# Performance work log

Measured on AMD Instinct MI355X. Metric: run time of the kernel, lower is better.

Reference implementation:

```python
import jax, jax.numpy as jnp
import numpy as np

N_AGENTS = 8
HID = 256            # hidden_size == comm_dim
COMP = 32            # composition_dim
VOCAB = 256          # vocab_size (table has VOCAB+1 rows, last row = EOS token)
T = HID // COMP      # total_tokens = 8
EPSILON = 1e-6
NF = 1.0 / np.sqrt(HID)  # norm_factor


def setup_inputs() -> dict:
    key = jax.random.key(0)
    ks = jax.random.split(key, 12)
    B = 2048 * N_AGENTS  # n_rollout_threads * num_agents
    s = 0.05
    return {
        "hidden_state": jax.random.normal(ks[0], (B, HID), jnp.float32),
        "eps": jax.random.normal(ks[1], (T, B, COMP), jnp.float32),
        "W_Q": jax.random.normal(ks[2], (HID, HID), jnp.float32) * s,
        "b_Q": jnp.zeros((HID,), jnp.float32),
        "W_K": jax.random.normal(ks[3], (HID, HID), jnp.float32) * s,
        "b_K": jnp.zeros((HID,), jnp.float32),
        "W_mu": jax.random.normal(ks[4], (HID, COMP), jnp.float32) * s,
        "b_mu": jnp.zeros((COMP,), jnp.float32),
        "W_var": jax.random.normal(ks[5], (HID, COMP), jnp.float32) * s,
        "b_var": jnp.zeros((COMP,), jnp.float32),
        "vocab": jax.random.uniform(ks[6], (VOCAB + 1, COMP), jnp.float32, minval=-2.0, maxval=2.0),
        "W_sum": jax.random.normal(ks[7], (HID, HID), jnp.float32) * s,
        "b_sum": jnp.zeros((HID,), jnp.float32),
        "W_head": jax.random.normal(ks[8], (HID, HID), jnp.float32) * s,
        "b_head": jnp.zeros((HID,), jnp.float32),
    }


def _forward(hidden_state, eps, W_Q, b_Q, W_K, b_K, W_mu, b_mu, W_var, b_var,
             vocab, W_sum, b_sum, W_head, b_head):
    B = hidden_state.shape[0]
    # NOTE: original code sets V = to_K(hidden_state) (to_V is unused) -- kept faithfully.
    Q = (hidden_state @ W_Q + b_Q) * NF            # [B, HID]
    V = hidden_state @ W_K + b_K                   # [B, HID]
    EOS = vocab[-1]                                # [COMP]

    message = jnp.zeros((B, T, COMP), hidden_state.dtype)
    mask = jnp.ones((B,), hidden_state.dtype)
    finished = jnp.zeros((B,), bool)

    # Sequential recurrence over a small fixed number of tokens (T = 8).
    for i in range(T):
        m = message.reshape(B, HID)
        K = (m @ W_K + b_K) * NF                   # [B, HID]
        attn = jax.nn.softmax(-(Q * K), axis=-1)   # softmin == softmax of negated logits
        hidden_attn = attn * V                     # [B, HID]
        token_mu = hidden_attn @ W_mu + b_mu       # [B, COMP]
        token_log_var = hidden_attn @ W_var + b_var
        token = eps[i] * jnp.exp(0.5 * token_log_var) + token_mu
        # per-dimension min of squared distance over all vocab entries (faithful to torch.min(.,1)[0])
        token = jnp.min((token[:, None, :] - vocab) ** 2, axis=1)  # [B, COMP]
        token = token * mask[:, None]
        eos_hit = jnp.sum((token - EOS) ** 2, axis=-1) < EPSILON   # [B]
        if i > 0:
            prev_hit = jnp.any(
                jnp.sum((token[:, None, :] - message[:, :i]) ** 2, axis=-1) < EPSILON, axis=1)
            hit = jnp.logical_or(prev_hit, eos_hit)
        else:
            hit = eos_hit
        new_eos = jnp.logical_and(hit, jnp.logical_not(finished))
        token = jnp.where(new_eos[:, None], EOS, token)
        mask = jnp.where(hit, jnp.zeros_like(mask), mask)
        finished = jnp.logical_or(finished, hit)
        message = message.at[:, i].set(token)

    comm = message.reshape(B, HID)                 # comm_dim == HID
    b = B // N_AGENTS
    comm = comm.reshape(b, N_AGENTS, HID) / (N_AGENTS - 1)  # comm_mode 'avg'
    # expand to [b, n, n, C] then sum over dim 1 == broadcast total sum to every agent
    comm_sum = jnp.broadcast_to(comm.sum(axis=1, keepdims=True), (b, N_AGENTS, HID))
    comm_sum = comm_sum.reshape(B, HID)
    out = comm_sum @ W_sum + b_sum                 # comm_sum_head
    out = jax.nn.relu(out @ W_head + b_head)       # active_func(comm_head(.))
    return out


def reference(hidden_state, eps, W_Q, b_Q, W_K, b_K, W_mu, b_mu, W_var, b_var,
              vocab, W_sum, b_sum, W_head, b_head):
    return _forward(hidden_state, eps, W_Q, b_Q, W_K, b_K, W_mu, b_mu, W_var, b_var,
                    vocab, W_sum, b_sum, W_head, b_head)
```

## Files before the change

kernel.cpp:

```cpp
#include <hip/hip_runtime.h>

#define ROWSB 32
#define HIDN 256
#define TT 8
#define EPSI 1e-6f
#define HAS 260
#define SVS 260
#define TBSTR 40
#define NCELL 128
#define WS_LUT_F   (32*SVS)
#define WS_DINFO_F (32*SVS + 2048)
#define WS_WMV_F   (32*SVS + 2048 + 64)

__device__ __forceinline__ void ld4(float* d, const float* p) {
  float4 v = *(const float4*)p;
  d[0] = v.x; d[1] = v.y; d[2] = v.z; d[3] = v.w;
}
__device__ __forceinline__ void ld2(float* d, const float* p) {
  float2 v = *(const float2*)p;
  d[0] = v.x; d[1] = v.y;
}
__device__ __forceinline__ void lds_fence() {
  asm volatile("s_waitcnt lgkmcnt(0)" ::: "memory");
}
__device__ __forceinline__ void fma8(float4 wv, float h0, float h1,
                                     float* mu0, float* lv0, float* mu1, float* lv1) {
  mu0[0] += h0*wv.x; lv0[0] += h0*wv.y; mu0[1] += h0*wv.z; lv0[1] += h0*wv.w;
  mu1[0] += h1*wv.x; lv1[0] += h1*wv.y; mu1[1] += h1*wv.z; lv1[1] += h1*wv.w;
}

__global__ __launch_bounds__(256)
void sort_vocab(const float* __restrict__ vocab,
                const float* __restrict__ Wmu, const float* __restrict__ Wvar,
                float* __restrict__ ws) {
  __shared__ float arr[512];
  const int d = blockIdx.x;
  const int t = threadIdx.x;
  ws[WS_WMV_F + ((size_t)t*32 + d)*2 + 0] = Wmu[(size_t)t*32 + d];
  ws[WS_WMV_F + ((size_t)t*32 + d)*2 + 1] = Wvar[(size_t)t*32 + d];
  arr[t] = (t < 257) ? vocab[t*32 + d] : 3.0e38f;
  arr[t+256] = (t == 0) ? vocab[256*32 + d] : 3.0e38f;
  __syncthreads();
  for (int k = 2; k <= 512; k <<= 1) {
    for (int j = k >> 1; j > 0; j >>= 1) {
      #pragma unroll
      for (int h = 0; h < 2; ++h) {
        int i = t + h*256;
        int ixj = i ^ j;
        if (ixj > i) {
          float a = arr[i], b = arr[ixj];
          bool up = ((i & k) == 0);
          if ((a > b) == up) { arr[i] = b; arr[ixj] = a; }
        }
      }
      __syncthreads();
    }
  }
  #pragma unroll
  for (int h = 0; h < 2; ++h) {
    int i = t + h*256;
    if (i < SVS) ws[d*SVS + i] = (i < 257) ? arr[i] : 3.0e38f;
  }
  float base = arr[0];
  float maxv = arr[256];
  float scale = (float)NCELL / fmaxf(maxv - base, 1e-30f);
  if (t == 0) {
    float2* dinfo = (float2*)(ws + WS_DINFO_F);
    dinfo[d] = make_float2(base, scale);
  }
  if (t < NCELL) {
    float target = base + (float)t * (maxv - base) * (1.0f/(float)NCELL);
    int lo = 0, hi = 257;
    while (lo < hi) { int mid = (lo+hi)>>1; if (arr[mid] < target) lo = mid+1; else hi = mid; }
    ((unsigned short*)(ws + WS_LUT_F))[d*NCELL + t] = (unsigned short)lo;
  }
}

__global__ __launch_bounds__(256, 2)
void mac_fused(const float* __restrict__ hs, const float* __restrict__ eps,
               const float* __restrict__ WQ, const float* __restrict__ bQ,
               const float* __restrict__ WK, const float* __restrict__ bK,
               const float* __restrict__ Wmu, const float* __restrict__ bmu,
               const float* __restrict__ Wvar, const float* __restrict__ bvar,
               const float* __restrict__ vocab,
               const float* __restrict__ Wsum, const float* __restrict__ bsum,
               const float* __restrict__ Whead, const float* __restrict__ bhead,
               const float* __restrict__ ws, float* __restrict__ out, int Btot)
{
  __shared__ __align__(16) float ha[ROWSB*HAS];
  __shared__ __align__(16) float sV[32*SVS];
  __shared__ __align__(16) unsigned short lut[32*NCELL];
  __shared__ __align__(16) float tokbuf[ROWSB*TBSTR];
  __shared__ float ivbuf[ROWSB], finbuf[ROWSB];

  const int t   = threadIdx.x;
  const int c4  = t & 63;
  const int w   = t >> 6;
  const int rp  = t >> 4;
  const int dp  = t & 15;
  const int d0u = (c4 << 2) & 31;
  const int tg  = c4 >> 3;
  const int rowbase = blockIdx.x * ROWSB;

  float Qr[8][4], Vr[8][4], Kr[8][4], MSGr[8][4];
  float eosv[4];
  unsigned fin = 0u;

  {
    const float* hp = hs + (size_t)(rowbase + w*8)*HIDN + c4*4;
    #pragma unroll
    for (int rr = 0; rr < 8; ++rr)
      *(float4*)&ha[(w*8+rr)*HAS + c4*4] = *(const float4*)(hp + (size_t)rr*HIDN);
  }
  for (int i = t; i < 32*SVS/4; i += 256)
    *(float4*)&sV[i*4] = *(const float4*)(ws + (size_t)i*4);
  for (int i = t; i < 512; i += 256)
    ((float4*)lut)[i] = ((const float4*)(ws + WS_LUT_F))[i];
  if (c4 < 8) finbuf[w*8 + c4] = 0.f;
  ld4(eosv, vocab + 256*32 + d0u);
  {
    float bq[4], bk[4];
    ld4(bq, bQ + c4*4); ld4(bk, bK + c4*4);
    #pragma unroll
    for (int rr = 0; rr < 8; ++rr) {
      #pragma unroll
      for (int k = 0; k < 4; ++k) { Qr[rr][k] = bq[k]; Vr[rr][k] = bk[k]; }
    }
  }
  float dbr[2], dsr[2];
  {
    float t0[4];
    ld4(t0, ws + WS_DINFO_F + dp*4);
    dbr[0]=t0[0]; dsr[0]=t0[1]; dbr[1]=t0[2]; dsr[1]=t0[3];
  }
  float bm[2], bv[2];
  ld2(bm, bmu + dp*2); ld2(bv, bvar + dp*2);
  lds_fence();

  #pragma unroll 2
  for (int jq = 0; jq < 64; ++jq) {
    float hsq[8][4];
    #pragma unroll
    for (int rr = 0; rr < 8; ++rr) ld4(hsq[rr], &ha[(w*8+rr)*HAS + jq*4]);
    #pragma unroll
    for (int m = 0; m < 4; ++m) {
      float wq[4], wk[4];
      ld4(wq, WQ + (size_t)(jq*4+m)*HIDN + c4*4);
      ld4(wk, WK + (size_t)(jq*4+m)*HIDN + c4*4);
      #pragma unroll
      for (int rr = 0; rr < 8; ++rr) {
        #pragma unroll
        for (int k = 0; k < 4; ++k) {
          Qr[rr][k] += hsq[rr][m]*wq[k];
          Vr[rr][k] += hsq[rr][m]*wk[k];
        }
      }
    }
  }
  {
    float bk[4]; ld4(bk, bK + c4*4);
    #pragma unroll
    for (int rr = 0; rr < 8; ++rr) {
      #pragma unroll
      for (int k = 0; k < 4; ++k) {
        Qr[rr][k] *= (1.0f/256.0f);
        Kr[rr][k]   = bk[k];
        MSGr[rr][k] = 0.f;
      }
    }
  }

  __syncthreads();

  for (int it = 0; it < TT; ++it) {
    if (it > 0) {
      const float* Wr = WK + (size_t)((it-1)*32)*HIDN + c4*4;
      #pragma unroll 2
      for (int cq = 0; cq < 8; ++cq) {
        float tq[8][4];
        #pragma unroll
        for (int rr = 0; rr < 8; ++rr) ld4(tq[rr], &tokbuf[(w*8+rr)*TBSTR + cq*4]);
        #pragma unroll
        for (int m = 0; m < 4; ++m) {
          float wv[4]; ld4(wv, Wr + (size_t)(cq*4+m)*HIDN);
          #pragma unroll
          for (int rr = 0; rr < 8; ++rr) {
            #pragma unroll
            for (int k = 0; k < 4; ++k) Kr[rr][k] += tq[rr][m]*wv[k];
          }
        }
      }
    }

    float ep0[2], ep1[2];
    ld2(ep0, eps + ((size_t)it*Btot + rowbase + 2*rp)*32 + dp*2);
    ld2(ep1, eps + ((size_t)it*Btot + rowbase + 2*rp+1)*32 + dp*2);

    #pragma unroll
    for (int rr = 0; rr < 8; ++rr) {
      float e[4]; float s = 0.f;
      #pragma unroll
      for (int k = 0; k < 4; ++k) { e[k] = __expf(-(Qr[rr][k]*Kr[rr][k])); s += e[k]; }
      #pragma unroll
      for (int off = 32; off >= 1; off >>= 1) s += __shfl_xor(s, off);
      if (c4 == rr) ivbuf[w*8+rr] = 1.0f / s;
      *(float4*)&ha[(w*8+rr)*HAS + c4*4] =
          make_float4(e[0]*Vr[rr][0], e[1]*Vr[rr][1], e[2]*Vr[rr][2], e[3]*Vr[rr][3]);
    }
    lds_fence();

    float mu0[2]={0,0}, lv0[2]={0,0}, mu1[2]={0,0}, lv1[2]={0,0};
    {
      const float* wmv  = ws + WS_WMV_F + dp*4;
      const float* har0 = &ha[(2*rp)*HAS];
      const float* har1 = &ha[(2*rp+1)*HAS];
      float4 wb0[8], wb1[8];
      #pragma unroll
      for (int u = 0; u < 8; ++u) wb0[u] = *(const float4*)(wmv + (size_t)u*64);
      #pragma unroll 1
      for (int bb = 0; bb < 16; ++bb) {
        {
          const int b = 2*bb;
          float4 h0a = *(const float4*)(har0 + b*8);
          float4 h1a = *(const float4*)(har1 + b*8);
          float4 h0b = *(const float4*)(har0 + b*8 + 4);
          float4 h1b = *(const float4*)(har1 + b*8 + 4);
          const float* wp = wmv + (size_t)(b+1)*512;
          #pragma unroll
          for (int u = 0; u < 8; ++u) wb1[u] = *(const float4*)(wp + (size_t)u*64);
          fma8(wb0[0], h0a.x, h1a.x, mu0, lv0, mu1, lv1);
          fma8(wb0[1], h0a.y, h1a.y, mu0, lv0, mu1, lv1);
          fma8(wb0[2], h0a.z, h1a.z, mu0, lv0, mu1, lv1);
          fma8(wb0[3], h0a.w, h1a.w, mu0, lv0, mu1, lv1);
          fma8(wb0[4], h0b.x, h1b.x, mu0, lv0, mu1, lv1);
          fma8(wb0[5], h0b.y, h1b.y, mu0, lv0, mu1, lv1);
          fma8(wb0[6], h0b.z, h1b.z, mu0, lv0, mu1, lv1);
          fma8(wb0[7], h0b.w, h1b.w, mu0, lv0, mu1, lv1);
        }
        {
          const int b = 2*bb+1;
          float4 h0a = *(const float4*)(har0 + b*8);
          float4 h1a = *(const float4*)(har1 + b*8);
          float4 h0b = *(const float4*)(har0 + b*8 + 4);
          float4 h1b = *(const float4*)(har1 + b*8 + 4);
          if (bb < 15) {
            const float* wp = wmv + (size_t)(b+1)*512;
            #pragma unroll
            for (int u = 0; u < 8; ++u) wb0[u] = *(const float4*)(wp + (size_t)u*64);
          }
          fma8(wb1[0], h0a.x, h1a.x, mu0, lv0, mu1, lv1);
          fma8(wb1[1], h0a.y, h1a.y, mu0, lv0, mu1, lv1);
          fma8(wb1[2], h0a.z, h1a.z, mu0, lv0, mu1, lv1);
          fma8(wb1[3], h0a.w, h1a.w, mu0, lv0, mu1, lv1);
          fma8(wb1[4], h0b.x, h1b.x, mu0, lv0, mu1, lv1);
          fma8(wb1[5], h0b.y, h1b.y, mu0, lv0, mu1, lv1);
          fma8(wb1[6], h0b.z, h1b.z, mu0, lv0, mu1, lv1);
          fma8(wb1[7], h0b.w, h1b.w, mu0, lv0, mu1, lv1);
        }
      }
    }
    {
      float ivr0 = ivbuf[2*rp],  ivr1 = ivbuf[2*rp+1];
      float msk0 = 1.0f - finbuf[2*rp], msk1 = 1.0f - finbuf[2*rp+1];
      float md0[2], md1[2];
      #pragma unroll
      for (int d = 0; d < 2; ++d) {
        const int dim = 2*dp + d;
        const float* sp = &sV[dim*SVS];
        {
          float mu = mu0[d]*ivr0 + bm[d];
          float lv = lv0[d]*ivr0 + bv[d];
          float x  = ep0[d]*__expf(0.5f*lv) + mu;
          int c = (int)((x - dbr[d]) * dsr[d]);
          c = min(max(c, 0), NCELL-1);
          int idx = (int)lut[dim*NCELL + c];
          float v = sp[idx];
          while (v < x) { ++idx; v = sp[idx]; }
          float dn = v - x;
          float dpv = (idx > 0) ? (x - sp[idx-1]) : 3.0e38f;
          md0[d] = fminf(dn, dpv);
        }
        {
          float mu = mu1[d]*ivr1 + bm[d];
          float lv = lv1[d]*ivr1 + bv[d];
          float x  = ep1[d]*__expf(0.5f*lv) + mu;
          int c = (int)((x - dbr[d]) * dsr[d]);
          c = min(max(c, 0), NCELL-1);
          int idx = (int)lut[dim*NCELL + c];
          float v = sp[idx];
          while (v < x) { ++idx; v = sp[idx]; }
          float dn = v - x;
          float dpv = (idx > 0) ? (x - sp[idx-1]) : 3.0e38f;
          md1[d] = fminf(dn, dpv);
        }
      }
      *(float2*)&tokbuf[(2*rp)*TBSTR + dp*2]   = make_float2(md0[0]*md0[0]*msk0, md0[1]*md0[1]*msk0);
      *(float2*)&tokbuf[(2*rp+1)*TBSTR + dp*2] = make_float2(md1[0]*md1[0]*msk1, md1[1]*md1[1]*msk1);
    }
    lds_fence();

    {
      float tokr[8][4];
      #pragma unroll
      for (int rr = 0; rr < 8; ++rr) ld4(tokr[rr], &tokbuf[(w*8+rr)*TBSTR + d0u]);
      unsigned newfin = fin;
      #pragma unroll
      for (int rr = 0; rr < 8; ++rr) {
        float pd = 0.f, ed = 0.f;
        #pragma unroll
        for (int k = 0; k < 4; ++k) { float dm = tokr[rr][k]-MSGr[rr][k]; pd += dm*dm; }
        if (tg == 0) {
          #pragma unroll
          for (int k = 0; k < 4; ++k) { float de = tokr[rr][k]-eosv[k]; ed += de*de; }
        }
        pd += __shfl_xor(pd, 1); ed += __shfl_xor(ed, 1);
        pd += __shfl_xor(pd, 2); ed += __shfl_xor(ed, 2);
        pd += __shfl_xor(pd, 4); ed += __shfl_xor(ed, 4);
        bool lane_hit = (tg < it && pd < EPSI) || (tg == 0 && ed < EPSI);
        bool hit = (__ballot(lane_hit) != 0ull);
        if (hit) {
          if ((tg == it) && !((fin >> rr) & 1u)) {
            #pragma unroll
            for (int k = 0; k < 4; ++k) tokr[rr][k] = eosv[k];
          }
          newfin |= (1u << rr);
        }
        if (tg == it) {
          #pragma unroll
          for (int k = 0; k < 4; ++k) MSGr[rr][k] = tokr[rr][k];
        }
      }
      if (tg == it) {
        #pragma unroll
        for (int rr = 0; rr < 8; ++rr)
          *(float4*)&tokbuf[(w*8+rr)*TBSTR + d0u] =
              make_float4(MSGr[rr][0], MSGr[rr][1], MSGr[rr][2], MSGr[rr][3]);
      }
      if (c4 < 8) finbuf[w*8+c4] = ((newfin >> c4) & 1u) ? 1.f : 0.f;
      fin = newfin;
    }
    lds_fence();
  }

  __syncthreads();
  float* commb = ha;
  float* o1    = ha + 4*HAS;
  {
    float cs[4] = {0,0,0,0};
    #pragma unroll
    for (int rr = 0; rr < 8; ++rr) {
      #pragma unroll
      for (int k = 0; k < 4; ++k) cs[k] += MSGr[rr][k];
    }
    const float i7 = 1.0f/7.0f;
    *(float4*)&commb[w*HAS + c4*4] = make_float4(cs[0]*i7, cs[1]*i7, cs[2]*i7, cs[3]*i7);
  }
  __syncthreads();
  {
    float bs = bsum[t];
    float a1[4] = {bs, bs, bs, bs};
    #pragma unroll 2
    for (int jq = 0; jq < 64; ++jq) {
      float w4[4];
      #pragma unroll
      for (int m = 0; m < 4; ++m) w4[m] = Wsum[(size_t)(jq*4+m)*HIDN + t];
      #pragma unroll
      for (int g = 0; g < 4; ++g) {
        float c[4]; ld4(c, &commb[g*HAS + jq*4]);
        a1[g] += c[0]*w4[0] + c[1]*w4[1] + c[2]*w4[2] + c[3]*w4[3];
      }
    }
    #pragma unroll
    for (int g = 0; g < 4; ++g) o1[g*HAS + t] = a1[g];
  }
  __syncthreads();
  {
    float bh = bhead[t];
    float a2[4] = {bh, bh, bh, bh};
    #pragma unroll 2
    for (int jq = 0; jq < 64; ++jq) {
      float w4[4];
      #pragma unroll
      for (int m = 0; m < 4; ++m) w4[m] = Whead[(size_t)(jq*4+m)*HIDN + t];
      #pragma unroll
      for (int g = 0; g < 4; ++g) {
        float c[4]; ld4(c, &o1[g*HAS + jq*4]);
        a2[g] += c[0]*w4[0] + c[1]*w4[1] + c[2]*w4[2] + c[3]*w4[3];
      }
    }
    #pragma unroll
    for (int g = 0; g < 4; ++g) {
      float r = fmaxf(a2[g], 0.f);
      #pragma unroll
      for (int rr = 0; rr < 8; ++rr)
        out[(size_t)(rowbase + g*8 + rr)*HIDN + t] = r;
    }
  }
}

extern "C" void kernel_launch(void* const* d_in, const int* in_sizes, int n_in,
                              void* d_out, int out_size, void* d_ws, size_t ws_size,
                              hipStream_t stream) {
    const float* hs    = (const float*)d_in[0];
    const float* eps   = (const float*)d_in[1];
    const float* WQ    = (const float*)d_in[2];
    const float* bQ    = (const float*)d_in[3];
    const float* WK    = (const float*)d_in[4];
    const float* bK    = (const float*)d_in[5];
    const float* Wmu   = (const float*)d_in[6];
    const float* bmu   = (const float*)d_in[7];
    const float* Wvar  = (const float*)d_in[8];
    const float* bvar  = (const float*)d_in[9];
    const float* vocab = (const float*)d_in[10];
    const float* Wsum  = (const float*)d_in[11];
    const float* bsum  = (const float*)d_in[12];
    const float* Whead = (const float*)d_in[13];
    const float* bhead = (const float*)d_in[14];
    float* o = (float*)d_out;
    float* wsf = (float*)d_ws;
    int Btot = in_sizes[0] / HIDN;
    hipLaunchKernelGGL(sort_vocab, dim3(32), dim3(256), 0, stream, vocab, Wmu, Wvar, wsf);
    hipLaunchKernelGGL(mac_fused, dim3(Btot / ROWSB), dim3(256), 0, stream,
                       hs, eps, WQ, bQ, WK, bK, Wmu, bmu, Wvar, bvar,
                       vocab, Wsum, bsum, Whead, bhead, wsf, o, Btot);
}
```

Before: 424.8 us.

## Move sorted vocab and LUT to global memory, spill V to LDS

The per-block shared copies of the sorted vocab columns and the lookup table are dropped, and the nearest-neighbour search now reads them from global memory (cache-resident). The LUT grows from 128 to 512 cells so the linear scan after the lookup is shorter. The V projection is no longer held in registers across the recurrence; it is written to a new LDS buffer and reloaded each iteration, which frees registers. A __syncthreads is replaced by an lgkmcnt wait. The aim is lower register and LDS pressure and higher occupancy, at the cost of global-memory latency in the search loop and extra LDS traffic.

```diff
diff --git a/kernel.cpp b/kernel.cpp
--- a/kernel.cpp
+++ b/kernel.cpp
@@ -7,10 +7,10 @@
 #define HAS 260
 #define SVS 260
 #define TBSTR 40
-#define NCELL 128
+#define NCELL 512
 #define WS_LUT_F   (32*SVS)
-#define WS_DINFO_F (32*SVS + 2048)
-#define WS_WMV_F   (32*SVS + 2048 + 64)
+#define WS_DINFO_F (32*SVS + 8192)
+#define WS_WMV_F   (32*SVS + 8192 + 64)
 
 __device__ __forceinline__ void ld4(float* d, const float* p) {
   float4 v = *(const float4*)p;
@@ -68,11 +68,13 @@
     float2* dinfo = (float2*)(ws + WS_DINFO_F);
     dinfo[d] = make_float2(base, scale);
   }
-  if (t < NCELL) {
-    float target = base + (float)t * (maxv - base) * (1.0f/(float)NCELL);
+  #pragma unroll
+  for (int h = 0; h < 2; ++h) {
+    int cell = t + h*256;
+    float target = base + (float)cell * (maxv - base) * (1.0f/(float)NCELL);
     int lo = 0, hi = 257;
     while (lo < hi) { int mid = (lo+hi)>>1; if (arr[mid] < target) lo = mid+1; else hi = mid; }
-    ((unsigned short*)(ws + WS_LUT_F))[d*NCELL + t] = (unsigned short)lo;
+    ((unsigned short*)(ws + WS_LUT_F))[d*NCELL + cell] = (unsigned short)lo;
   }
 }
 
@@ -88,8 +90,7 @@
                const float* __restrict__ ws, float* __restrict__ out, int Btot)
 {
   __shared__ __align__(16) float ha[ROWSB*HAS];
-  __shared__ __align__(16) float sV[32*SVS];
-  __shared__ __align__(16) unsigned short lut[32*NCELL];
+  __shared__ __align__(16) float vbuf[ROWSB*HAS];
   __shared__ __align__(16) float tokbuf[ROWSB*TBSTR];
   __shared__ float ivbuf[ROWSB], finbuf[ROWSB];
 
@@ -102,7 +103,7 @@
   const int tg  = c4 >> 3;
   const int rowbase = blockIdx.x * ROWSB;
 
-  float Qr[8][4], Vr[8][4], Kr[8][4], MSGr[8][4];
+  float Qr[8][4], Kr[8][4], MSGr[8][4];
   float eosv[4];
   unsigned fin = 0u;
 
@@ -112,21 +113,8 @@
     for (int rr = 0; rr < 8; ++rr)
       *(float4*)&ha[(w*8+rr)*HAS + c4*4] = *(const float4*)(hp + (size_t)rr*HIDN);
   }
-  for (int i = t; i < 32*SVS/4; i += 256)
-    *(float4*)&sV[i*4] = *(const float4*)(ws + (size_t)i*4);
-  for (int i = t; i < 512; i += 256)
-    ((float4*)lut)[i] = ((const float4*)(ws + WS_LUT_F))[i];
   if (c4 < 8) finbuf[w*8 + c4] = 0.f;
   ld4(eosv, vocab + 256*32 + d0u);
-  {
-    float bq[4], bk[4];
-    ld4(bq, bQ + c4*4); ld4(bk, bK + c4*4);
-    #pragma unroll
-    for (int rr = 0; rr < 8; ++rr) {
-      #pragma unroll
-      for (int k = 0; k < 4; ++k) { Qr[rr][k] = bq[k]; Vr[rr][k] = bk[k]; }
-    }
-  }
   float dbr[2], dsr[2];
   {
     float t0[4];
@@ -137,25 +125,41 @@
   ld2(bm, bmu + dp*2); ld2(bv, bvar + dp*2);
   lds_fence();
 
-  #pragma unroll 2
-  for (int jq = 0; jq < 64; ++jq) {
-    float hsq[8][4];
-    #pragma unroll
-    for (int rr = 0; rr < 8; ++rr) ld4(hsq[rr], &ha[(w*8+rr)*HAS + jq*4]);
-    #pragma unroll
-    for (int m = 0; m < 4; ++m) {
-      float wq[4], wk[4];
-      ld4(wq, WQ + (size_t)(jq*4+m)*HIDN + c4*4);
-      ld4(wk, WK + (size_t)(jq*4+m)*HIDN + c4*4);
+  {
+    float Vr[8][4];
+    {
+      float bq[4], bk[4];
+      ld4(bq, bQ + c4*4); ld4(bk, bK + c4*4);
       #pragma unroll
       for (int rr = 0; rr < 8; ++rr) {
         #pragma unroll
-        for (int k = 0; k < 4; ++k) {
-          Qr[rr][k] += hsq[rr][m]*wq[k];
-          Vr[rr][k] += hsq[rr][m]*wk[k];
-        }
-      }
-    }
+        for (int k = 0; k < 4; ++k) { Qr[rr][k] = bq[k]; Vr[rr][k] = bk[k]; }
+      }
+    }
+    #pragma unroll 2
+    for (int jq = 0; jq < 64; ++jq) {
+      float hsq[8][4];
+      #pragma unroll
+      for (int rr = 0; rr < 8; ++rr) ld4(hsq[rr], &ha[(w*8+rr)*HAS + jq*4]);
+      #pragma unroll
+      for (int m = 0; m < 4; ++m) {
+        float wq[4], wk[4];
+        ld4(wq, WQ + (size_t)(jq*4+m)*HIDN + c4*4);
+        ld4(wk, WK + (size_t)(jq*4+m)*HIDN + c4*4);
+        #pragma unroll
+        for (int rr = 0; rr < 8; ++rr) {
+          #pragma unroll
+          for (int k = 0; k < 4; ++k) {
+            Qr[rr][k] += hsq[rr][m]*wq[k];
+            Vr[rr][k] += hsq[rr][m]*wk[k];
+          }
+        }
+      }
+    }
+    #pragma unroll
+    for (int rr = 0; rr < 8; ++rr)
+      *(float4*)&vbuf[(w*8+rr)*HAS + c4*4] =
+          make_float4(Vr[rr][0], Vr[rr][1], Vr[rr][2], Vr[rr][3]);
   }
   {
     float bk[4]; ld4(bk, bK + c4*4);
@@ -169,8 +173,7 @@
       }
     }
   }
-
-  __syncthreads();
+  lds_fence();
 
   for (int it = 0; it < TT; ++it) {
     if (it > 0) {
@@ -204,8 +207,10 @@
       #pragma unroll
       for (int off = 32; off >= 1; off >>= 1) s += __shfl_xor(s, off);
       if (c4 == rr) ivbuf[w*8+rr] = 1.0f / s;
+      float vv[4];
+      ld4(vv, &vbuf[(w*8+rr)*HAS + c4*4]);
       *(float4*)&ha[(w*8+rr)*HAS + c4*4] =
-          make_float4(e[0]*Vr[rr][0], e[1]*Vr[rr][1], e[2]*Vr[rr][2], e[3]*Vr[rr][3]);
+          make_float4(e[0]*vv[0], e[1]*vv[1], e[2]*vv[2], e[3]*vv[3]);
     }
     lds_fence();
 
@@ -262,18 +267,19 @@
     {
       float ivr0 = ivbuf[2*rp],  ivr1 = ivbuf[2*rp+1];
       float msk0 = 1.0f - finbuf[2*rp], msk1 = 1.0f - finbuf[2*rp+1];
+      const unsigned short* lutg = (const unsigned short*)(ws + WS_LUT_F);
       float md0[2], md1[2];
       #pragma unroll
       for (int d = 0; d < 2; ++d) {
         const int dim = 2*dp + d;
-        const float* sp = &sV[dim*SVS];
+        const float* sp = ws + dim*SVS;
         {
           float mu = mu0[d]*ivr0 + bm[d];
           float lv = lv0[d]*ivr0 + bv[d];
           float x  = ep0[d]*__expf(0.5f*lv) + mu;
           int c = (int)((x - dbr[d]) * dsr[d]);
           c = min(max(c, 0), NCELL-1);
-          int idx = (int)lut[dim*NCELL + c];
+          int idx = (int)lutg[dim*NCELL + c];
           float v = sp[idx];
           while (v < x) { ++idx; v = sp[idx]; }
           float dn = v - x;
@@ -286,7 +292,7 @@
           float x  = ep1[d]*__expf(0.5f*lv) + mu;
           int c = (int)((x - dbr[d]) * dsr[d]);
           c = min(max(c, 0), NCELL-1);
-          int idx = (int)lut[dim*NCELL + c];
+          int idx = (int)lutg[dim*NCELL + c];
           float v = sp[idx];
           while (v < x) { ++idx; v = sp[idx]; }
           float dn = v - x;
```

Measured after the change: 391.3 us. 1.09x faster.
